# Optimization experiments

Hardware: AMD Instinct MI355X
Metric: run time of the kernel (lower is better)

Reference implementation:

```python
import jax, jax.numpy as jnp
import numpy as np

B, T, C = 16, 2048, 64

def setup_inputs() -> dict:
    key = jax.random.key(0)
    x = jax.random.normal(key, (B, T, C), dtype=jnp.float32)
    # learned scalar params (as in build()): r_sigma init 0.01, margin init 0.0
    r_sigma = jnp.array([0.01], dtype=jnp.float32)
    margin = jnp.array([0.0], dtype=jnp.float32)
    return {"x": x, "r_sigma": r_sigma, "margin": margin}

def reference(x, r_sigma, margin):
    # Pairwise squared euclidean distances via the gram trick:
    # ||xi - xj||^2 = ||xi||^2 + ||xj||^2 - 2 xi.xj  (mathematically identical
    # to the original diff -> norm -> square, but avoids the (B,T,T,C) tensor
    # and the non-differentiable sqrt(0) on the diagonal).
    _, size, _ = x.shape
    sq = jnp.sum(x * x, axis=-1)                              # (B,T)
    gram = jnp.einsum('btc,bsc->bts', x, x)                   # (B,T,T)
    sqdist = jnp.maximum(sq[:, :, None] + sq[:, None, :] - 2.0 * gram, 0.0)
    # Gaussian kernel with learned inverse-bandwidth and margin
    Kmat = jnp.exp(-sqdist * r_sigma[0] + margin[0])          # (B,T,T)
    # off-diagonal mask (zero self-similarity)
    Kmat = Kmat * (1.0 - jnp.eye(size, dtype=x.dtype))
    # residual kernel attention: x + K @ x
    return x + jnp.einsum('bts,bsc->btc', Kmat, x)
```

## Files before the change

### kernel.cpp

```cpp
#include <hip/hip_runtime.h>
#include <stdint.h>
#include <stddef.h>

#define BB 16
#define TT 2048
#define CC 64

typedef __attribute__((ext_vector_type(8))) short short8;
typedef __attribute__((ext_vector_type(4))) short s16x4;
typedef __attribute__((ext_vector_type(4))) float f32x4;
typedef __attribute__((ext_vector_type(16))) float f32x16;

#if defined(__has_builtin)
#if __has_builtin(__builtin_amdgcn_exp2f)
#define EXP2(x) __builtin_amdgcn_exp2f(x)
#else
#define EXP2(x) exp2f(x)
#endif
#else
#define EXP2(x) exp2f(x)
#endif

static __device__ __forceinline__ unsigned short f2bf(float f) {
  union { float f; unsigned int u; } v; v.f = f;
  unsigned int u = v.u;
  return (unsigned short)((u + 0x7FFFu + ((u >> 16) & 1u)) >> 16);
}

static __device__ __forceinline__ short8 pack_swap(
    float a0, float a1, float a2, float a3,
    float a4, float a5, float a6, float a7) {
  unsigned X, Z, Y, W;
  asm("v_cvt_pk_bf16_f32 %0, %1, %2" : "=v"(X) : "v"(a0), "v"(a1));
  asm("v_cvt_pk_bf16_f32 %0, %1, %2" : "=v"(Z) : "v"(a2), "v"(a3));
  asm("v_cvt_pk_bf16_f32 %0, %1, %2" : "=v"(Y) : "v"(a4), "v"(a5));
  asm("v_cvt_pk_bf16_f32 %0, %1, %2" : "=v"(W) : "v"(a6), "v"(a7));
  asm("v_permlane32_swap_b32 %0, %1" : "+v"(X), "+v"(Y));
  asm("v_permlane32_swap_b32 %0, %1" : "+v"(Z), "+v"(W));
  union { unsigned u[4]; short8 s; } u;
  u.u[0] = X; u.u[1] = Z; u.u[2] = Y; u.u[3] = W;
  return u.s;
}

__global__ __launch_bounds__(256, 4) void prep_kernel(
    const float* __restrict__ x, unsigned short* __restrict__ xb,
    unsigned short* __restrict__ xbT, float* __restrict__ sq)
{
  __shared__ unsigned short tile[16 * 68];
  const int b   = blockIdx.x >> 7;
  const int t0  = (blockIdx.x & 127) << 4;
  const int tid = threadIdx.x;
  const int r   = tid >> 4;
  const int cg  = tid & 15;
  const int c4  = cg * 4;

  const size_t idx = (size_t)(b * TT + t0 + r) * CC + c4;
  const f32x4 v = *(const f32x4*)(x + idx);
  float ssq = v[0]*v[0] + v[1]*v[1] + v[2]*v[2] + v[3]*v[3];

  s16x4 hv;
  hv[0] = (short)f2bf(v[0]); hv[1] = (short)f2bf(v[1]);
  hv[2] = (short)f2bf(v[2]); hv[3] = (short)f2bf(v[3]);
  *(s16x4*)(xb + idx) = hv;
  *(s16x4*)(&tile[r * 68 + c4]) = hv;

  ssq += __shfl_xor(ssq, 1); ssq += __shfl_xor(ssq, 2);
  ssq += __shfl_xor(ssq, 4); ssq += __shfl_xor(ssq, 8);
  if (cg == 0) sq[(size_t)b * TT + t0 + r] = ssq;
  __syncthreads();

  const int c = tid >> 2, tq = tid & 3;
  s16x4 o;
#pragma unroll
  for (int k = 0; k < 4; ++k) o[k] = (short)tile[(tq * 4 + k) * 68 + c];
  *(s16x4*)(xbT + (size_t)(b * CC + c) * TT + t0 + tq * 4) = o;
}

__global__ __launch_bounds__(256, 2) void attn_kernel(
    const float* __restrict__ x, const unsigned short* __restrict__ xb,
    const unsigned short* __restrict__ xbT, const float* __restrict__ sq,
    const float* __restrict__ rsig, const float* __restrict__ marg,
    float* __restrict__ out)
{
  __shared__ unsigned short Klds[2][64 * 64];
  __shared__ unsigned short Vlds[2][64 * 64];
  __shared__ float Red[2][32 * 64];

  const int bid = ((blockIdx.x & 7) << 6) | (blockIdx.x >> 3);
  const int b   = bid >> 5;
  const int qb  = (bid & 31) << 6;
  const int tid = threadIdx.x;
  const int w = tid >> 6, lane = tid & 63;
  const int l31 = lane & 31, hi1 = lane >> 5;
  const int wq = w & 1, ws = w >> 1;

  const float L2E = 1.44269504088896f;
  const float rl2 = -rsig[0] * L2E;
  const float ml2 = marg[0] * L2E;

  const unsigned short* xb_b  = xb  + (size_t)b * TT * CC;
  const unsigned short* xbT_b = xbT + (size_t)b * CC * TT;
  const float* sq_b = sq + (size_t)b * TT;

  const int q0w = qb + wq * 32;

  short8 qf[4];
#pragma unroll
  for (int kc = 0; kc < 4; ++kc)
    qf[kc] = *(const short8*)(xb_b + (size_t)(q0w + l31) * CC + kc * 16 + hi1 * 8);
  const float aq = sq_b[q0w + l31];

  f32x16 oacc[2];
#pragma unroll
  for (int ct = 0; ct < 2; ++ct)
#pragma unroll
    for (int i = 0; i < 16; ++i) oacc[ct][i] = 0.f;

  const int srow = tid >> 3, slot = tid & 7;
  const int swz0 = srow * 64        + ((slot ^ (srow & 7)) * 8);
  const int swz1 = (srow + 32) * 64 + ((slot ^ (srow & 7)) * 8);

  short8 stg0, stg1, stg2, stg3;
  auto LOADT = [&](int t) {
    const size_t sb = (size_t)t * 64;
    stg0 = *(const short8*)(xb_b  + (sb + srow) * CC + slot * 8);
    stg1 = *(const short8*)(xb_b  + (sb + 32 + srow) * CC + slot * 8);
    stg2 = *(const short8*)(xbT_b + (size_t)srow * TT + sb + slot * 8);
    stg3 = *(const short8*)(xbT_b + (size_t)(srow + 32) * TT + sb + slot * 8);
  };
  auto WRITET = [&](int bf) {
    *(short8*)(&Klds[bf][swz0]) = stg0;
    *(short8*)(&Klds[bf][swz1]) = stg1;
    *(short8*)(&Vlds[bf][swz0]) = stg2;
    *(short8*)(&Vlds[bf][swz1]) = stg3;
  };

  LOADT(0); WRITET(0);
  __syncthreads();

  const int rr = ws * 32 + l31;
  for (int t = 0; t < 32; ++t) {
    const int cur = t & 1;
    const int tb = t * 64;
    if (t + 1 < 32) LOADT(t + 1);

    float aqas[16];
#pragma unroll
    for (int r = 0; r < 16; ++r)
      aqas[r] = aq + sq_b[tb + ws * 32 + ((r & 3) + 8 * (r >> 2)) + 4 * hi1];

    f32x16 sac;
#pragma unroll
    for (int i = 0; i < 16; ++i) sac[i] = 0.f;
#pragma unroll
    for (int kc = 0; kc < 4; ++kc) {
      const short8 kf = *(const short8*)(
          &Klds[cur][rr * 64 + (((kc * 2 + hi1) ^ (rr & 7)) * 8)]);
      sac = __builtin_amdgcn_mfma_f32_32x32x16_bf16(kf, qf[kc], sac, 0, 0, 0);
    }

    float p[16];
#pragma unroll
    for (int r = 0; r < 16; ++r) {
      float d = fmaf(sac[r], -2.f, aqas[r]);
      d = fmaxf(d, 0.f);
      p[r] = EXP2(fmaf(d, rl2, ml2));
    }
    if (tb + ws * 32 == qb + wq * 32) {
#pragma unroll
      for (int r = 0; r < 16; ++r) {
        const int sl = (r & 3) + 8 * (r >> 2) + 4 * hi1;
        if (sl == l31) p[r] = 0.f;
      }
    }

    short8 af0 = pack_swap(p[0], p[1], p[2],  p[3],  p[4],  p[5],  p[6],  p[7]);
    short8 af1 = pack_swap(p[8], p[9], p[10], p[11], p[12], p[13], p[14], p[15]);

#pragma unroll
    for (int ct = 0; ct < 2; ++ct) {
      const int rowc = ct * 32 + l31;
#pragma unroll
      for (int kk = 0; kk < 2; ++kk) {
        const short8 vf = *(const short8*)(
            &Vlds[cur][rowc * 64 + (((ws * 4 + kk * 2 + hi1) ^ (rowc & 7)) * 8)]);
        oacc[ct] = __builtin_amdgcn_mfma_f32_32x32x16_bf16(
            kk ? af1 : af0, vf, oacc[ct], 0, 0, 0);
      }
    }

    if (t + 1 < 32) WRITET(cur ^ 1);
    __syncthreads();
  }

  if (ws == 1) {
#pragma unroll
    for (int ct = 0; ct < 2; ++ct)
#pragma unroll
      for (int r = 0; r < 16; ++r) {
        const int ql = (r & 3) + 8 * (r >> 2) + 4 * hi1;
        Red[wq][ql * 64 + ct * 32 + l31] = oacc[ct][r];
      }
  }
  __syncthreads();
  if (ws == 0) {
#pragma unroll
    for (int ct = 0; ct < 2; ++ct)
#pragma unroll
      for (int r = 0; r < 16; ++r) {
        const int ql = (r & 3) + 8 * (r >> 2) + 4 * hi1;
        const int c  = ct * 32 + l31;
        const size_t idx = (size_t)(b * TT + qb + wq * 32 + ql) * CC + c;
        out[idx] = x[idx] + oacc[ct][r] + Red[wq][ql * 64 + c];
      }
  }
}

extern "C" void kernel_launch(void* const* d_in, const int* in_sizes, int n_in,
                              void* d_out, int out_size, void* d_ws, size_t ws_size,
                              hipStream_t stream) {
  const float* x    = (const float*)d_in[0];
  const float* rsig = (const float*)d_in[1];
  const float* marg = (const float*)d_in[2];
  float* out = (float*)d_out;

  unsigned short* xb  = (unsigned short*)d_ws;
  unsigned short* xbT = xb + (size_t)BB * TT * CC;
  float* sq = (float*)(xbT + (size_t)BB * TT * CC);

  prep_kernel<<<2048, 256, 0, stream>>>(x, xb, xbT, sq);
  attn_kernel<<<512, 256, 0, stream>>>(x, xb, xbT, sq, rsig, marg, out);
}
```

Baseline: 100.1 us.

## Load K/V fragments directly from global memory, dropping LDS staging and barriers

Removes the double-buffered LDS staging of K and V tiles and the per-iteration __syncthreads. Each wave now loads its MFMA operand fragments straight from global (L2-resident) bf16 buffers, and the squared norms are loaded as vector loads. The diagonal-mask check is precomputed outside the loop and the loop is unrolled by two. This trades LDS traffic and barrier stalls for redundant global/L2 loads across waves, with load latency exposed unless the unroll hides it.

```diff
diff --git a/kernel.cpp b/kernel.cpp
--- a/kernel.cpp
+++ b/kernel.cpp
@@ -82,8 +82,6 @@
     const float* __restrict__ rsig, const float* __restrict__ marg,
     float* __restrict__ out)
 {
-  __shared__ unsigned short Klds[2][64 * 64];
-  __shared__ unsigned short Vlds[2][64 * 64];
   __shared__ float Red[2][32 * 64];
 
   const int bid = ((blockIdx.x & 7) << 6) | (blockIdx.x >> 3);
@@ -116,57 +114,51 @@
 #pragma unroll
     for (int i = 0; i < 16; ++i) oacc[ct][i] = 0.f;
 
-  const int srow = tid >> 3, slot = tid & 7;
-  const int swz0 = srow * 64        + ((slot ^ (srow & 7)) * 8);
-  const int swz1 = (srow + 32) * 64 + ((slot ^ (srow & 7)) * 8);
-
-  short8 stg0, stg1, stg2, stg3;
-  auto LOADT = [&](int t) {
-    const size_t sb = (size_t)t * 64;
-    stg0 = *(const short8*)(xb_b  + (sb + srow) * CC + slot * 8);
-    stg1 = *(const short8*)(xb_b  + (sb + 32 + srow) * CC + slot * 8);
-    stg2 = *(const short8*)(xbT_b + (size_t)srow * TT + sb + slot * 8);
-    stg3 = *(const short8*)(xbT_b + (size_t)(srow + 32) * TT + sb + slot * 8);
-  };
-  auto WRITET = [&](int bf) {
-    *(short8*)(&Klds[bf][swz0]) = stg0;
-    *(short8*)(&Klds[bf][swz1]) = stg1;
-    *(short8*)(&Vlds[bf][swz0]) = stg2;
-    *(short8*)(&Vlds[bf][swz1]) = stg3;
-  };
-
-  LOADT(0); WRITET(0);
-  __syncthreads();
-
-  const int rr = ws * 32 + l31;
+  const unsigned short* kbase  = xb_b  + (size_t)(ws * 32 + l31) * CC + hi1 * 8;
+  const unsigned short* vbase0 = xbT_b + (size_t)(l31) * TT      + ws * 32 + hi1 * 8;
+  const unsigned short* vbase1 = xbT_b + (size_t)(32 + l31) * TT + ws * 32 + hi1 * 8;
+  const float* sqp = sq_b + ws * 32 + 4 * hi1;
+
+  const int dtile = (qb + wq * 32 - ws * 32) >> 6;
+  const bool dvalid = ((qb + wq * 32 - ws * 32) & 63) == 0 &&
+                      dtile >= 0 && dtile < 32;
+
+#pragma unroll 2
   for (int t = 0; t < 32; ++t) {
-    const int cur = t & 1;
     const int tb = t * 64;
-    if (t + 1 < 32) LOADT(t + 1);
-
-    float aqas[16];
-#pragma unroll
-    for (int r = 0; r < 16; ++r)
-      aqas[r] = aq + sq_b[tb + ws * 32 + ((r & 3) + 8 * (r >> 2)) + 4 * hi1];
+
+    short8 kf[4];
+#pragma unroll
+    for (int kc = 0; kc < 4; ++kc)
+      kf[kc] = *(const short8*)(kbase + (size_t)tb * CC + kc * 16);
+
+    f32x4 sqv[4];
+#pragma unroll
+    for (int ch = 0; ch < 4; ++ch)
+      sqv[ch] = *(const f32x4*)(sqp + tb + ch * 8);
+
+    short8 vf[2][2];
+#pragma unroll
+    for (int kk = 0; kk < 2; ++kk) {
+      vf[0][kk] = *(const short8*)(vbase0 + tb + kk * 16);
+      vf[1][kk] = *(const short8*)(vbase1 + tb + kk * 16);
+    }
 
     f32x16 sac;
 #pragma unroll
     for (int i = 0; i < 16; ++i) sac[i] = 0.f;
 #pragma unroll
-    for (int kc = 0; kc < 4; ++kc) {
-      const short8 kf = *(const short8*)(
-          &Klds[cur][rr * 64 + (((kc * 2 + hi1) ^ (rr & 7)) * 8)]);
-      sac = __builtin_amdgcn_mfma_f32_32x32x16_bf16(kf, qf[kc], sac, 0, 0, 0);
-    }
+    for (int kc = 0; kc < 4; ++kc)
+      sac = __builtin_amdgcn_mfma_f32_32x32x16_bf16(kf[kc], qf[kc], sac, 0, 0, 0);
 
     float p[16];
 #pragma unroll
     for (int r = 0; r < 16; ++r) {
-      float d = fmaf(sac[r], -2.f, aqas[r]);
+      float d = fmaf(sac[r], -2.f, aq + sqv[r >> 2][r & 3]);
       d = fmaxf(d, 0.f);
       p[r] = EXP2(fmaf(d, rl2, ml2));
     }
-    if (tb + ws * 32 == qb + wq * 32) {
+    if (dvalid && t == dtile) {
 #pragma unroll
       for (int r = 0; r < 16; ++r) {
         const int sl = (r & 3) + 8 * (r >> 2) + 4 * hi1;
@@ -174,23 +166,14 @@
       }
     }
 
-    short8 af0 = pack_swap(p[0], p[1], p[2],  p[3],  p[4],  p[5],  p[6],  p[7]);
-    short8 af1 = pack_swap(p[8], p[9], p[10], p[11], p[12], p[13], p[14], p[15]);
+    const short8 af0 = pack_swap(p[0], p[1], p[2],  p[3],  p[4],  p[5],  p[6],  p[7]);
+    const short8 af1 = pack_swap(p[8], p[9], p[10], p[11], p[12], p[13], p[14], p[15]);
 
 #pragma unroll
     for (int ct = 0; ct < 2; ++ct) {
-      const int rowc = ct * 32 + l31;
-#pragma unroll
-      for (int kk = 0; kk < 2; ++kk) {
-        const short8 vf = *(const short8*)(
-            &Vlds[cur][rowc * 64 + (((ws * 4 + kk * 2 + hi1) ^ (rowc & 7)) * 8)]);
-        oacc[ct] = __builtin_amdgcn_mfma_f32_32x32x16_bf16(
-            kk ? af1 : af0, vf, oacc[ct], 0, 0, 0);
-      }
-    }
-
-    if (t + 1 < 32) WRITET(cur ^ 1);
-    __syncthreads();
+      oacc[ct] = __builtin_amdgcn_mfma_f32_32x32x16_bf16(af0, vf[ct][0], oacc[ct], 0, 0, 0);
+      oacc[ct] = __builtin_amdgcn_mfma_f32_32x32x16_bf16(af1, vf[ct][1], oacc[ct], 0, 0, 0);
+    }
   }
 
   if (ws == 1) {
```

Result: slower. 135.2 us (+35.1%).

## Use 8 waves per block with 128-key tiles and staged sq in LDS

Applied to the files above, without the earlier changes.

Doubles the block to 512 threads so four wave groups split the key dimension, each handling 32 keys of a 128-key tile, which halves the number of loop iterations and barriers. Squared norms for the key tile are now staged in LDS alongside the K/V tiles instead of being read per lane from global memory. The final reduction sums partials from three extra wave groups through reused shared memory. The change brings a larger LDS footprint per block and a heavier reduction step, and the launch bounds now request more waves per CU.

```diff
diff --git a/kernel.cpp b/kernel.cpp
--- a/kernel.cpp
+++ b/kernel.cpp
@@ -5,6 +5,7 @@
 #define BB 16
 #define TT 2048
 #define CC 64
+#define NT 16
 
 typedef __attribute__((ext_vector_type(8))) short short8;
 typedef __attribute__((ext_vector_type(4))) short s16x4;
@@ -76,15 +77,14 @@
   *(s16x4*)(xbT + (size_t)(b * CC + c) * TT + t0 + tq * 4) = o;
 }
 
-__global__ __launch_bounds__(256, 2) void attn_kernel(
+__global__ __launch_bounds__(512, 4) void attn_kernel(
     const float* __restrict__ x, const unsigned short* __restrict__ xb,
     const unsigned short* __restrict__ xbT, const float* __restrict__ sq,
     const float* __restrict__ rsig, const float* __restrict__ marg,
     float* __restrict__ out)
 {
-  __shared__ unsigned short Klds[2][64 * 64];
-  __shared__ unsigned short Vlds[2][64 * 64];
-  __shared__ float Red[2][32 * 64];
+  __shared__ unsigned short SMEM[2][16384];
+  __shared__ float SqLds[2][128];
 
   const int bid = ((blockIdx.x & 7) << 6) | (blockIdx.x >> 3);
   const int b   = bid >> 5;
@@ -116,38 +116,50 @@
 #pragma unroll
     for (int i = 0; i < 16; ++i) oacc[ct][i] = 0.f;
 
-  const int srow = tid >> 3, slot = tid & 7;
-  const int swz0 = srow * 64        + ((slot ^ (srow & 7)) * 8);
-  const int swz1 = (srow + 32) * 64 + ((slot ^ (srow & 7)) * 8);
-
-  short8 stg0, stg1, stg2, stg3;
+  const int srowK = tid >> 3, slotK = tid & 7;
+  const int swzK  = srowK * 64 + ((slotK ^ (srowK & 7)) * 8);
+  const int srowV = tid >> 4, slotV = tid & 15;
+  const int swzV  = srowV * 128 + ((slotV ^ (srowV & 7)) * 8);
+
+  short8 sK0, sK1, sV0, sV1;
+  f32x4 sS;
   auto LOADT = [&](int t) {
-    const size_t sb = (size_t)t * 64;
-    stg0 = *(const short8*)(xb_b  + (sb + srow) * CC + slot * 8);
-    stg1 = *(const short8*)(xb_b  + (sb + 32 + srow) * CC + slot * 8);
-    stg2 = *(const short8*)(xbT_b + (size_t)srow * TT + sb + slot * 8);
-    stg3 = *(const short8*)(xbT_b + (size_t)(srow + 32) * TT + sb + slot * 8);
+    const size_t tb = (size_t)t * 128;
+    sK0 = *(const short8*)(xb_b + (tb + srowK) * CC + slotK * 8);
+    sK1 = *(const short8*)(xb_b + (tb + 64 + srowK) * CC + slotK * 8);
+    sV0 = *(const short8*)(xbT_b + (size_t)srowV * TT + tb + slotV * 8);
+    sV1 = *(const short8*)(xbT_b + (size_t)(srowV + 32) * TT + tb + slotV * 8);
+    if (tid < 32) sS = *(const f32x4*)(sq_b + tb + tid * 4);
   };
   auto WRITET = [&](int bf) {
-    *(short8*)(&Klds[bf][swz0]) = stg0;
-    *(short8*)(&Klds[bf][swz1]) = stg1;
-    *(short8*)(&Vlds[bf][swz0]) = stg2;
-    *(short8*)(&Vlds[bf][swz1]) = stg3;
+    unsigned short* Kp = &SMEM[bf][0];
+    unsigned short* Vp = &SMEM[bf][8192];
+    *(short8*)(&Kp[swzK])            = sK0;
+    *(short8*)(&Kp[swzK + 64 * 64])  = sK1;
+    *(short8*)(&Vp[swzV])            = sV0;
+    *(short8*)(&Vp[swzV + 32 * 128]) = sV1;
+    if (tid < 32) *(f32x4*)(&SqLds[bf][tid * 4]) = sS;
   };
 
   LOADT(0); WRITET(0);
   __syncthreads();
 
-  const int rr = ws * 32 + l31;
-  for (int t = 0; t < 32; ++t) {
+  const int rk = ws * 32 + l31;
+  const int dQ = q0w - ws * 32;
+  const int dtile  = dQ >> 7;
+  const bool dvalid = ((dQ & 127) == 0) && dtile >= 0 && dtile < NT;
+
+  for (int t = 0; t < NT; ++t) {
     const int cur = t & 1;
-    const int tb = t * 64;
-    if (t + 1 < 32) LOADT(t + 1);
-
-    float aqas[16];
-#pragma unroll
-    for (int r = 0; r < 16; ++r)
-      aqas[r] = aq + sq_b[tb + ws * 32 + ((r & 3) + 8 * (r >> 2)) + 4 * hi1];
+    if (t + 1 < NT) LOADT(t + 1);
+
+    const unsigned short* Kp = &SMEM[cur][0];
+    const unsigned short* Vp = &SMEM[cur][8192];
+
+    f32x4 sqv[4];
+#pragma unroll
+    for (int ch = 0; ch < 4; ++ch)
+      sqv[ch] = *(const f32x4*)(&SqLds[cur][ws * 32 + ch * 8 + 4 * hi1]);
 
     f32x16 sac;
 #pragma unroll
@@ -155,18 +167,18 @@
 #pragma unroll
     for (int kc = 0; kc < 4; ++kc) {
       const short8 kf = *(const short8*)(
-          &Klds[cur][rr * 64 + (((kc * 2 + hi1) ^ (rr & 7)) * 8)]);
+          &Kp[rk * 64 + (((kc * 2 + hi1) ^ (rk & 7)) * 8)]);
       sac = __builtin_amdgcn_mfma_f32_32x32x16_bf16(kf, qf[kc], sac, 0, 0, 0);
     }
 
     float p[16];
 #pragma unroll
     for (int r = 0; r < 16; ++r) {
-      float d = fmaf(sac[r], -2.f, aqas[r]);
+      float d = fmaf(sac[r], -2.f, aq + sqv[r >> 2][r & 3]);
       d = fmaxf(d, 0.f);
       p[r] = EXP2(fmaf(d, rl2, ml2));
     }
-    if (tb + ws * 32 == qb + wq * 32) {
+    if (dvalid && t == dtile) {
 #pragma unroll
       for (int r = 0; r < 16; ++r) {
         const int sl = (r & 3) + 8 * (r >> 2) + 4 * hi1;
@@ -174,32 +186,34 @@
       }
     }
 
-    short8 af0 = pack_swap(p[0], p[1], p[2],  p[3],  p[4],  p[5],  p[6],  p[7]);
-    short8 af1 = pack_swap(p[8], p[9], p[10], p[11], p[12], p[13], p[14], p[15]);
+    const short8 af0 = pack_swap(p[0], p[1], p[2],  p[3],  p[4],  p[5],  p[6],  p[7]);
+    const short8 af1 = pack_swap(p[8], p[9], p[10], p[11], p[12], p[13], p[14], p[15]);
 
 #pragma unroll
     for (int ct = 0; ct < 2; ++ct) {
-      const int rowc = ct * 32 + l31;
+      const int rc = ct * 32 + l31;
 #pragma unroll
       for (int kk = 0; kk < 2; ++kk) {
         const short8 vf = *(const short8*)(
-            &Vlds[cur][rowc * 64 + (((ws * 4 + kk * 2 + hi1) ^ (rowc & 7)) * 8)]);
+            &Vp[rc * 128 + (((ws * 4 + kk * 2 + hi1) ^ (rc & 7)) * 8)]);
         oacc[ct] = __builtin_amdgcn_mfma_f32_32x32x16_bf16(
             kk ? af1 : af0, vf, oacc[ct], 0, 0, 0);
       }
     }
 
-    if (t + 1 < 32) WRITET(cur ^ 1);
+    if (t + 1 < NT) WRITET(cur ^ 1);
     __syncthreads();
   }
 
-  if (ws == 1) {
+  float* RedF = (float*)&SMEM[0][0];
+  if (ws != 0) {
+    const int base = ((ws - 1) * 2 + wq) * 2048;
 #pragma unroll
     for (int ct = 0; ct < 2; ++ct)
 #pragma unroll
       for (int r = 0; r < 16; ++r) {
         const int ql = (r & 3) + 8 * (r >> 2) + 4 * hi1;
-        Red[wq][ql * 64 + ct * 32 + l31] = oacc[ct][r];
+        RedF[base + ql * 64 + ct * 32 + l31] = oacc[ct][r];
       }
   }
   __syncthreads();
@@ -210,8 +224,12 @@
       for (int r = 0; r < 16; ++r) {
         const int ql = (r & 3) + 8 * (r >> 2) + 4 * hi1;
         const int c  = ct * 32 + l31;
+        const int off = ql * 64 + c;
         const size_t idx = (size_t)(b * TT + qb + wq * 32 + ql) * CC + c;
-        out[idx] = x[idx] + oacc[ct][r] + Red[wq][ql * 64 + c];
+        out[idx] = x[idx] + oacc[ct][r]
+                 + RedF[(0 * 2 + wq) * 2048 + off]
+                 + RedF[(1 * 2 + wq) * 2048 + off]
+                 + RedF[(2 * 2 + wq) * 2048 + off];
       }
   }
 }
@@ -229,5 +247,5 @@
   float* sq = (float*)(xbT + (size_t)BB * TT * CC);
 
   prep_kernel<<<2048, 256, 0, stream>>>(x, xb, xbT, sq);
-  attn_kernel<<<512, 256, 0, stream>>>(x, xb, xbT, sq, rsig, marg, out);
-}
+  attn_kernel<<<512, 512, 0, stream>>>(x, xb, xbT, sq, rsig, marg, out);
+}
```

Result: slower. 110.0 us (+9.9%).
